# Kernel optimization log

Hardware: AMD Instinct MI355X
Metric: run time of the kernel (lower is better)

## Reference

```python
import jax, jax.numpy as jnp
import numpy as np

DIM = 768
N_HEADS = 12
HEAD_DIM = DIM // N_HEADS
HIDDEN = int(DIM * 4.0)
B, S = 4, 2048
EPS = 1e-6
SCALE = HEAD_DIM ** -0.5


def layer_norm(x, gamma, beta):
    mu = jnp.mean(x, axis=-1, keepdims=True)
    var = jnp.mean((x - mu) ** 2, axis=-1, keepdims=True)
    return (x - mu) * jax.lax.rsqrt(var + EPS) * gamma + beta


def setup_inputs() -> dict:
    key = jax.random.key(0)
    ks = jax.random.split(key, 8)
    x = jax.random.normal(ks[0], (B, S, DIM), dtype=jnp.float32)
    mask = jax.random.randint(ks[1], (B, 1, S, S), 0, 2, dtype=jnp.int32)
    sd = DIM ** -0.5
    return {
        "x": x,
        "mask": mask,
        "w_qkv": jax.random.normal(ks[2], (DIM, 3 * DIM), dtype=jnp.float32) * sd,
        "b_qkv": jnp.zeros((3 * DIM,), jnp.float32),
        "w_proj": jax.random.normal(ks[3], (DIM, DIM), dtype=jnp.float32) * sd,
        "b_proj": jnp.zeros((DIM,), jnp.float32),
        "g1": jnp.ones((DIM,), jnp.float32),
        "beta1": jnp.zeros((DIM,), jnp.float32),
        "g2": jnp.ones((DIM,), jnp.float32),
        "beta2": jnp.zeros((DIM,), jnp.float32),
        "w1": jax.random.normal(ks[4], (DIM, HIDDEN), dtype=jnp.float32) * sd,
        "b1": jnp.zeros((HIDDEN,), jnp.float32),
        "w2": jax.random.normal(ks[5], (HIDDEN, DIM), dtype=jnp.float32) * (HIDDEN ** -0.5),
        "b2": jnp.zeros((DIM,), jnp.float32),
    }


def reference(x, mask, w_qkv, b_qkv, w_proj, b_proj, g1, beta1, g2, beta2, w1, b1, w2, b2):
    # --- attention branch (pre-LN) ---
    h = layer_norm(x, g1, beta1)
    qkv = h @ w_qkv + b_qkv                              # (B,S,3*DIM)
    qkv = qkv.reshape(B, S, 3, N_HEADS, HEAD_DIM)
    q, k, v = (qkv[:, :, 0], qkv[:, :, 1], qkv[:, :, 2])  # (B,S,H,D)
    # scores: (B,H,S,S) -- materialized like the original
    dp = jnp.einsum("bqhd,bkhd->bhqk", q, k) * SCALE
    dp = jnp.where(mask == 0, jnp.float32(-10000.0), dp)
    attn = jax.nn.softmax(dp, axis=-1)
    wa = jnp.einsum("bhqk,bkhd->bqhd", attn, v).reshape(B, S, DIM)
    x = x + (wa @ w_proj + b_proj)
    # --- MLP branch (pre-LN) ---
    h = layer_norm(x, g2, beta2)
    h = jax.nn.gelu(h @ w1 + b1, approximate=False)
    x = x + (h @ w2 + b2)
    return x
```

## Files before the change

kernel.cpp:

```cpp
#include <hip/hip_runtime.h>
#include <hip/hip_bf16.h>
#include <math.h>

typedef __bf16 bf16;
typedef __bf16 bf16x8 __attribute__((ext_vector_type(8)));
typedef short bf16x4s __attribute__((ext_vector_type(4)));
typedef float f32x4 __attribute__((ext_vector_type(4)));

#define DIM 768
#define NH 12
#define HD 64
#define HID 3072
#define BB 4
#define SS 2048
#define SCALE_QK 0.125f
#define QPRESCALE 0.18033688011112042f

#define MFMA(a, b, c) __builtin_amdgcn_mfma_f32_16x16x32_bf16(a, b, c, 0, 0, 0)
#define MFMA16(a, b, c) \
  __builtin_amdgcn_mfma_f32_16x16x16bf16_1k(a, b, c, 0, 0, 0)

__device__ __forceinline__ void gld16(const void* g, void* l) {
  __builtin_amdgcn_global_load_lds(
      (const __attribute__((address_space(1))) void*)g,
      (__attribute__((address_space(3))) void*)l, 16, 0, 0);
}

__device__ __forceinline__ unsigned pk2(float a, float b) {
  union {
    bf16 h[2];
    unsigned u;
  } t;
  t.h[0] = (bf16)a;
  t.h[1] = (bf16)b;
  return t.u;
}

__global__ __launch_bounds__(256) void castT_all_kernel(
    const float* __restrict__ s0, bf16* __restrict__ d0,
    const float* __restrict__ s1, bf16* __restrict__ d1,
    const float* __restrict__ s2, bf16* __restrict__ d2,
    const float* __restrict__ s3, bf16* __restrict__ d3) {
  __shared__ float tile[32][33];
  int id = blockIdx.x;
  const float* in;
  bf16* out;
  int R, C, loc;
  if (id < 1728) { in = s0; out = d0; R = 768; C = 2304; loc = id; }
  else if (id < 2304) { in = s1; out = d1; R = 768; C = 768; loc = id - 1728; }
  else if (id < 4608) { in = s2; out = d2; R = 768; C = 3072; loc = id - 2304; }
  else { in = s3; out = d3; R = 3072; C = 768; loc = id - 4608; }
  const int cb = C >> 5;
  const int c0 = (loc % cb) * 32, r0 = (loc / cb) * 32;
  const int tx = threadIdx.x & 31, ty = threadIdx.x >> 5;
#pragma unroll
  for (int i = 0; i < 32; i += 8)
    tile[ty + i][tx] = in[(size_t)(r0 + ty + i) * C + c0 + tx];
  __syncthreads();
#pragma unroll
  for (int i = 0; i < 32; i += 8)
    out[(size_t)(c0 + ty + i) * R + r0 + tx] = (bf16)tile[tx][ty + i];
}

__global__ __launch_bounds__(256) void maskbits_kernel(
    const int* __restrict__ mask, unsigned* __restrict__ bits) {
  const int i = blockIdx.x * 256 + threadIdx.x;
  unsigned long long m = __ballot(mask[i] != 0);
  const int lane = threadIdx.x & 63;
  if (lane == 0) bits[i >> 5] = (unsigned)m;
  else if (lane == 32) bits[i >> 5] = (unsigned)(m >> 32);
}

__global__ __launch_bounds__(256) void ln_kernel(
    const float* __restrict__ x, const float* __restrict__ g,
    const float* __restrict__ beta, bf16* __restrict__ out) {
  const int row = blockIdx.x, t = threadIdx.x;
  const float* xr = x + (size_t)row * DIM;
  float v0 = xr[t], v1 = xr[t + 256], v2 = xr[t + 512];
  float s = v0 + v1 + v2;
  float s2 = v0 * v0 + v1 * v1 + v2 * v2;
#pragma unroll
  for (int d = 1; d < 64; d <<= 1) {
    s += __shfl_xor(s, d);
    s2 += __shfl_xor(s2, d);
  }
  __shared__ float red[8];
  const int wv = t >> 6, lane = t & 63;
  if (lane == 0) { red[wv] = s; red[wv + 4] = s2; }
  __syncthreads();
  s = red[0] + red[1] + red[2] + red[3];
  s2 = red[4] + red[5] + red[6] + red[7];
  const float mu = s * (1.0f / DIM);
  const float var = s2 * (1.0f / DIM) - mu * mu;
  const float r = rsqrtf(var + 1e-6f);
  bf16* o = out + (size_t)row * DIM;
  o[t] = (bf16)((v0 - mu) * r * g[t] + beta[t]);
  o[t + 256] = (bf16)((v1 - mu) * r * g[t + 256] + beta[t + 256]);
  o[t + 512] = (bf16)((v2 - mu) * r * g[t + 512] + beta[t + 512]);
}

enum { EPI_QKV = 0, EPI_PROJ = 1, EPI_FFN1 = 2, EPI_FFN2 = 3 };

template <int EPI, int K>
__global__ __launch_bounds__(256) void gemm_kernel(
    const bf16* __restrict__ A, const bf16* __restrict__ Bt,
    const float* __restrict__ bias, const float* __restrict__ res,
    void* __restrict__ o0, void* __restrict__ o1, void* __restrict__ o2) {
  __shared__ bf16 As[128 * 64];
  __shared__ bf16 Bs[128 * 64];
  const int tid = threadIdx.x;
  const int wv = tid >> 6, lane = tid & 63;
  const int quad = lane >> 4, l15 = lane & 15;
  const int lrow = lane >> 3, lcol = lane & 7;
  const int m0 = blockIdx.y * 128, n0 = blockIdx.x * 128;
  const int wm = (wv >> 1) * 64, wn = (wv & 1) * 64;

  f32x4 acc[4][4] = {};

  const int swz = (lcol ^ lrow) * 8;
  const bf16* Ag = A + (size_t)(m0 + wv * 32 + lrow) * K + swz;
  const bf16* Bg = Bt + (size_t)(n0 + wv * 32 + lrow) * K + swz;
  bf16* Al = As + (wv * 32) * 64;
  bf16* Bl = Bs + (wv * 32) * 64;

  for (int k0 = 0; k0 < K; k0 += 64) {
#pragma unroll
    for (int i = 0; i < 4; i++) {
      gld16(Ag + (size_t)(i * 8) * K + k0, Al + i * 8 * 64);
      gld16(Bg + (size_t)(i * 8) * K + k0, Bl + i * 8 * 64);
    }
    __syncthreads();
#pragma unroll
    for (int ks = 0; ks < 2; ks++) {
      bf16x8 af[4], bfr[4];
#pragma unroll
      for (int i = 0; i < 4; i++) {
        const int ra = wm + i * 16 + l15;
        af[i] = *(const bf16x8*)&As[ra * 64 + ((ks * 4 + quad) ^ (ra & 7)) * 8];
        const int rb = wn + i * 16 + l15;
        bfr[i] = *(const bf16x8*)&Bs[rb * 64 + ((ks * 4 + quad) ^ (rb & 7)) * 8];
      }
#pragma unroll
      for (int mi = 0; mi < 4; mi++)
#pragma unroll
        for (int ni = 0; ni < 4; ni++)
          acc[mi][ni] = MFMA(af[mi], bfr[ni], acc[mi][ni]);
    }
    __syncthreads();
  }

#pragma unroll
  for (int mi = 0; mi < 4; mi++) {
#pragma unroll
    for (int ni = 0; ni < 4; ni++) {
      const int n = n0 + wn + ni * 16 + l15;
      const float bv = bias[n];
      const int mb = m0 + wm + mi * 16 + quad * 4;
      float val[4];
#pragma unroll
      for (int r = 0; r < 4; r++) val[r] = acc[mi][ni][r] + bv;
      if (EPI == EPI_QKV) {
        const int which = n / 768;
        const int nn = n - which * 768;
        const int hh = nn >> 6, d = nn & 63;
        const int bb = mb >> 11, s = mb & 2047;
        if (which == 0) {
#pragma unroll
          for (int r = 0; r < 4; r++)
            ((bf16*)o0)[((size_t)(bb * NH + hh) * SS + s + r) * HD + d] =
                (bf16)(val[r] * QPRESCALE);
        } else if (which == 1) {
#pragma unroll
          for (int r = 0; r < 4; r++)
            ((bf16*)o1)[((size_t)(bb * NH + hh) * SS + s + r) * HD + d] =
                (bf16)val[r];
        } else {
          uint2 pv;
          pv.x = pk2(val[0], val[1]);
          pv.y = pk2(val[2], val[3]);
          *(uint2*)&((bf16*)o2)[((size_t)(bb * NH + hh) * HD + d) * SS + s] = pv;
        }
      } else if (EPI == EPI_PROJ) {
#pragma unroll
        for (int r = 0; r < 4; r++)
          ((float*)o0)[(size_t)(mb + r) * DIM + n] =
              res[(size_t)(mb + r) * DIM + n] + val[r];
      } else if (EPI == EPI_FFN1) {
#pragma unroll
        for (int r = 0; r < 4; r++) {
          const float ge =
              0.5f * val[r] * (1.0f + erff(val[r] * 0.70710678118654752f));
          ((bf16*)o0)[(size_t)(mb + r) * HID + n] = (bf16)ge;
        }
      } else {
#pragma unroll
        for (int r = 0; r < 4; r++)
          ((float*)o0)[(size_t)(mb + r) * DIM + n] =
              res[(size_t)(mb + r) * DIM + n] + val[r];
      }
    }
  }
}

__global__ __launch_bounds__(256) void attn_kernel(
    const bf16* __restrict__ q, const bf16* __restrict__ k,
    const bf16* __restrict__ vT, const unsigned* __restrict__ bits,
    bf16* __restrict__ wa) {
  const int b = blockIdx.z, h = blockIdx.y, q0 = blockIdx.x * 128;
  const int tid = threadIdx.x, wv = tid >> 6, lane = tid & 63;
  const int quad = lane >> 4, l15 = lane & 15;
  const int lrow = lane >> 3, lcol = lane & 7;

  __shared__ bf16 Ks[64 * 64];
  __shared__ bf16 Vs[64 * 64];

  const bf16* qbh = q + (size_t)(b * NH + h) * SS * HD;
  const bf16* kbh = k + (size_t)(b * NH + h) * SS * HD;
  const bf16* vbh = vT + (size_t)(b * NH + h) * HD * SS;

  bf16x8 aq[2][2];
#pragma unroll
  for (int mi = 0; mi < 2; mi++)
#pragma unroll
    for (int ks = 0; ks < 2; ks++) {
      const int s = q0 + wv * 32 + mi * 16 + l15;
      aq[mi][ks] = *(const bf16x8*)&qbh[(size_t)s * HD + ks * 32 + quad * 8];
    }

  const unsigned long long* mptr[2];
#pragma unroll
  for (int mi = 0; mi < 2; mi++)
    mptr[mi] = (const unsigned long long*)bits +
               (size_t)(b * SS + q0 + wv * 32 + mi * 16 + l15) * 32;

  float lsum[2] = {0.0f, 0.0f};
  f32x4 O[2][4] = {};

  const int swz = (lcol ^ lrow) * 8;

  for (int s0 = 0; s0 < SS; s0 += 64) {
#pragma unroll
    for (int i = 0; i < 2; i++) {
      const int r = wv * 16 + i * 8 + lrow;
      gld16(&kbh[(size_t)(s0 + r) * HD + swz], &Ks[(wv * 16 + i * 8) * 64]);
      gld16(&vbh[(size_t)r * SS + s0 + swz], &Vs[(wv * 16 + i * 8) * 64]);
    }
    const unsigned long long ww[2] = {mptr[0][s0 >> 6] >> (quad * 4),
                                      mptr[1][s0 >> 6] >> (quad * 4)};
    __syncthreads();

    bf16x8 kf[4][2];
#pragma unroll
    for (int ni = 0; ni < 4; ni++)
#pragma unroll
      for (int ks = 0; ks < 2; ks++) {
        const int rr = ni * 16 + l15;
        kf[ni][ks] =
            *(const bf16x8*)&Ks[rr * 64 + ((ks * 4 + quad) ^ (rr & 7)) * 8];
      }
    bf16x4s vf[4][4];
#pragma unroll
    for (int nd = 0; nd < 4; nd++)
#pragma unroll
      for (int ni = 0; ni < 4; ni++) {
        const int row = nd * 16 + l15;
        const int pc = ((ni * 2 + (quad >> 1)) ^ (row & 7));
        vf[nd][ni] =
            *(const bf16x4s*)&Vs[row * 64 + pc * 8 + (quad & 1) * 4];
      }

    unsigned pf[2][4][2];
#pragma unroll
    for (int mi = 0; mi < 2; mi++) {
      const unsigned long long sh = ww[mi];
      float ls = lsum[mi];
#pragma unroll
      for (int ni = 0; ni < 4; ni++) {
        f32x4 a = {};
        a = MFMA(kf[ni][0], aq[mi][0], a);
        a = MFMA(kf[ni][1], aq[mi][1], a);
        float pv[4];
#pragma unroll
        for (int r = 0; r < 4; r++) {
          const unsigned bit = (unsigned)(sh >> (ni * 16 + r)) & 1u;
          const float p = bit ? __builtin_amdgcn_exp2f(a[r]) : 0.0f;
          pv[r] = p;
          ls += p;
        }
        pf[mi][ni][0] = pk2(pv[0], pv[1]);
        pf[mi][ni][1] = pk2(pv[2], pv[3]);
      }
      lsum[mi] = ls;
    }

#pragma unroll
    for (int mi = 0; mi < 2; mi++)
#pragma unroll
      for (int nd = 0; nd < 4; nd++)
#pragma unroll
        for (int ni = 0; ni < 4; ni++) {
          union {
            unsigned u[2];
            bf16x4s v;
          } pp;
          pp.u[0] = pf[mi][ni][0];
          pp.u[1] = pf[mi][ni][1];
          O[mi][nd] = MFMA16(vf[nd][ni], pp.v, O[mi][nd]);
        }
    __syncthreads();
  }

#pragma unroll
  for (int mi = 0; mi < 2; mi++) {
    float ls = lsum[mi];
    ls += __shfl_xor(ls, 16);
    ls += __shfl_xor(ls, 32);
    const float rln = __builtin_amdgcn_rcpf(ls);
    const int s = q0 + wv * 32 + mi * 16 + l15;
    bf16* dst = wa + (size_t)(b * SS + s) * DIM + h * HD + quad * 4;
#pragma unroll
    for (int nd = 0; nd < 4; nd++) {
      uint2 pv;
      pv.x = pk2(O[mi][nd][0] * rln, O[mi][nd][1] * rln);
      pv.y = pk2(O[mi][nd][2] * rln, O[mi][nd][3] * rln);
      *(uint2*)&dst[nd * 16] = pv;
    }
  }
}

extern "C" void kernel_launch(void* const* d_in, const int* in_sizes, int n_in,
                              void* d_out, int out_size, void* d_ws,
                              size_t ws_size, hipStream_t stream) {
  const float* x = (const float*)d_in[0];
  const int* mask = (const int*)d_in[1];
  const float* w_qkv = (const float*)d_in[2];
  const float* b_qkv = (const float*)d_in[3];
  const float* w_proj = (const float*)d_in[4];
  const float* b_proj = (const float*)d_in[5];
  const float* g1 = (const float*)d_in[6];
  const float* beta1 = (const float*)d_in[7];
  const float* g2 = (const float*)d_in[8];
  const float* beta2 = (const float*)d_in[9];
  const float* w1 = (const float*)d_in[10];
  const float* b1 = (const float*)d_in[11];
  const float* w2 = (const float*)d_in[12];
  const float* b2 = (const float*)d_in[13];
  float* out = (float*)d_out;

  char* p = (char*)d_ws;
  auto alloc = [&](size_t bytes) {
    char* r = p;
    p += (bytes + 1023) & ~(size_t)1023;
    return r;
  };
  bf16* wqkvT = (bf16*)alloc((size_t)2304 * 768 * 2);
  bf16* wprojT = (bf16*)alloc((size_t)768 * 768 * 2);
  bf16* w1T = (bf16*)alloc((size_t)3072 * 768 * 2);
  bf16* w2T = (bf16*)alloc((size_t)768 * 3072 * 2);
  unsigned* bits = (unsigned*)alloc((size_t)BB * SS * 64 * 4);
  bf16* h = (bf16*)alloc((size_t)8192 * 768 * 2);
  bf16* qb = (bf16*)alloc((size_t)8192 * 768 * 2);
  bf16* kb = (bf16*)alloc((size_t)8192 * 768 * 2);
  bf16* vtb = (bf16*)alloc((size_t)8192 * 768 * 2);
  bf16* wab = (bf16*)alloc((size_t)8192 * 768 * 2);
  float* x2 = (float*)alloc((size_t)8192 * 768 * 4);
  bf16* ffn1 = (bf16*)alloc((size_t)8192 * 3072 * 2);

  castT_all_kernel<<<6912, 256, 0, stream>>>(w_qkv, wqkvT, w_proj, wprojT, w1,
                                             w1T, w2, w2T);
  maskbits_kernel<<<(BB * SS * SS) / 256, 256, 0, stream>>>(mask, bits);
  ln_kernel<<<8192, 256, 0, stream>>>(x, g1, beta1, h);
  gemm_kernel<EPI_QKV, 768><<<dim3(2304 / 128, 8192 / 128), 256, 0, stream>>>(
      h, wqkvT, b_qkv, nullptr, qb, kb, vtb);
  attn_kernel<<<dim3(SS / 128, NH, BB), 256, 0, stream>>>(qb, kb, vtb, bits, wab);
  gemm_kernel<EPI_PROJ, 768><<<dim3(768 / 128, 8192 / 128), 256, 0, stream>>>(
      wab, wprojT, b_proj, x, x2, nullptr, nullptr);
  ln_kernel<<<8192, 256, 0, stream>>>(x2, g2, beta2, h);
  gemm_kernel<EPI_FFN1, 768><<<dim3(3072 / 128, 8192 / 128), 256, 0, stream>>>(
      h, w1T, b1, nullptr, ffn1, nullptr, nullptr);
  gemm_kernel<EPI_FFN2, 3072><<<dim3(768 / 128, 8192 / 128), 256, 0, stream>>>(
      ffn1, w2T, b2, x2, out, nullptr, nullptr);
}
```

Measured before the change: 497.7 us.

## Shrink attention query tile, compute row sums via MFMA, use 64-wide GEMM tiles

```diff
diff --git a/kernel.cpp b/kernel.cpp
--- a/kernel.cpp
+++ b/kernel.cpp
@@ -13,7 +13,6 @@
 #define HID 3072
 #define BB 4
 #define SS 2048
-#define SCALE_QK 0.125f
 #define QPRESCALE 0.18033688011112042f
 
 #define MFMA(a, b, c) __builtin_amdgcn_mfma_f32_16x16x32_bf16(a, b, c, 0, 0, 0)
@@ -101,47 +100,53 @@
 
 enum { EPI_QKV = 0, EPI_PROJ = 1, EPI_FFN1 = 2, EPI_FFN2 = 3 };
 
-template <int EPI, int K>
+template <int EPI, int K, int TN>
 __global__ __launch_bounds__(256) void gemm_kernel(
     const bf16* __restrict__ A, const bf16* __restrict__ Bt,
     const float* __restrict__ bias, const float* __restrict__ res,
     void* __restrict__ o0, void* __restrict__ o1, void* __restrict__ o2) {
+  constexpr int MI = (TN == 128) ? 4 : 2;
   __shared__ bf16 As[128 * 64];
-  __shared__ bf16 Bs[128 * 64];
+  __shared__ bf16 Bs[TN * 64];
   const int tid = threadIdx.x;
   const int wv = tid >> 6, lane = tid & 63;
   const int quad = lane >> 4, l15 = lane & 15;
   const int lrow = lane >> 3, lcol = lane & 7;
-  const int m0 = blockIdx.y * 128, n0 = blockIdx.x * 128;
-  const int wm = (wv >> 1) * 64, wn = (wv & 1) * 64;
-
-  f32x4 acc[4][4] = {};
+  const int m0 = blockIdx.y * 128, n0 = blockIdx.x * TN;
+  const int wm = (TN == 128) ? (wv >> 1) * 64 : wv * 32;
+  const int wn = (TN == 128) ? (wv & 1) * 64 : 0;
+
+  f32x4 acc[MI][4] = {};
 
   const int swz = (lcol ^ lrow) * 8;
   const bf16* Ag = A + (size_t)(m0 + wv * 32 + lrow) * K + swz;
-  const bf16* Bg = Bt + (size_t)(n0 + wv * 32 + lrow) * K + swz;
+  const bf16* Bg = Bt + (size_t)(n0 + wv * (TN / 4) + lrow) * K + swz;
   bf16* Al = As + (wv * 32) * 64;
-  bf16* Bl = Bs + (wv * 32) * 64;
+  bf16* Bl = Bs + (wv * (TN / 4)) * 64;
 
   for (int k0 = 0; k0 < K; k0 += 64) {
 #pragma unroll
-    for (int i = 0; i < 4; i++) {
+    for (int i = 0; i < 4; i++)
       gld16(Ag + (size_t)(i * 8) * K + k0, Al + i * 8 * 64);
+#pragma unroll
+    for (int i = 0; i < TN / 32; i++)
       gld16(Bg + (size_t)(i * 8) * K + k0, Bl + i * 8 * 64);
-    }
     __syncthreads();
 #pragma unroll
     for (int ks = 0; ks < 2; ks++) {
-      bf16x8 af[4], bfr[4];
-#pragma unroll
-      for (int i = 0; i < 4; i++) {
+      bf16x8 af[MI], bfr[4];
+#pragma unroll
+      for (int i = 0; i < MI; i++) {
         const int ra = wm + i * 16 + l15;
         af[i] = *(const bf16x8*)&As[ra * 64 + ((ks * 4 + quad) ^ (ra & 7)) * 8];
+      }
+#pragma unroll
+      for (int i = 0; i < 4; i++) {
         const int rb = wn + i * 16 + l15;
         bfr[i] = *(const bf16x8*)&Bs[rb * 64 + ((ks * 4 + quad) ^ (rb & 7)) * 8];
       }
 #pragma unroll
-      for (int mi = 0; mi < 4; mi++)
+      for (int mi = 0; mi < MI; mi++)
 #pragma unroll
         for (int ni = 0; ni < 4; ni++)
           acc[mi][ni] = MFMA(af[mi], bfr[ni], acc[mi][ni]);
@@ -150,7 +155,7 @@
   }
 
 #pragma unroll
-  for (int mi = 0; mi < 4; mi++) {
+  for (int mi = 0; mi < MI; mi++) {
 #pragma unroll
     for (int ni = 0; ni < 4; ni++) {
       const int n = n0 + wn + ni * 16 + l15;
@@ -206,36 +211,39 @@
     const bf16* __restrict__ q, const bf16* __restrict__ k,
     const bf16* __restrict__ vT, const unsigned* __restrict__ bits,
     bf16* __restrict__ wa) {
-  const int b = blockIdx.z, h = blockIdx.y, q0 = blockIdx.x * 128;
+  const int b = blockIdx.z, h = blockIdx.y, q0 = blockIdx.x * 64;
   const int tid = threadIdx.x, wv = tid >> 6, lane = tid & 63;
   const int quad = lane >> 4, l15 = lane & 15;
   const int lrow = lane >> 3, lcol = lane & 7;
 
   __shared__ bf16 Ks[64 * 64];
   __shared__ bf16 Vs[64 * 64];
+  __shared__ unsigned lut[32];
+
+  if (tid < 16) {
+    lut[2 * tid] =
+        ((tid & 1) ? 0xFFFFu : 0u) | ((tid & 2) ? 0xFFFF0000u : 0u);
+    lut[2 * tid + 1] =
+        ((tid & 4) ? 0xFFFFu : 0u) | ((tid & 8) ? 0xFFFF0000u : 0u);
+  }
 
   const bf16* qbh = q + (size_t)(b * NH + h) * SS * HD;
   const bf16* kbh = k + (size_t)(b * NH + h) * SS * HD;
   const bf16* vbh = vT + (size_t)(b * NH + h) * HD * SS;
 
-  bf16x8 aq[2][2];
-#pragma unroll
-  for (int mi = 0; mi < 2; mi++)
-#pragma unroll
-    for (int ks = 0; ks < 2; ks++) {
-      const int s = q0 + wv * 32 + mi * 16 + l15;
-      aq[mi][ks] = *(const bf16x8*)&qbh[(size_t)s * HD + ks * 32 + quad * 8];
-    }
-
-  const unsigned long long* mptr[2];
-#pragma unroll
-  for (int mi = 0; mi < 2; mi++)
-    mptr[mi] = (const unsigned long long*)bits +
-               (size_t)(b * SS + q0 + wv * 32 + mi * 16 + l15) * 32;
-
-  float lsum[2] = {0.0f, 0.0f};
-  f32x4 O[2][4] = {};
-
+  const int sq = q0 + wv * 16 + l15;
+  bf16x8 aq[2];
+#pragma unroll
+  for (int ks = 0; ks < 2; ks++)
+    aq[ks] = *(const bf16x8*)&qbh[(size_t)sq * HD + ks * 32 + quad * 8];
+
+  const unsigned long long* mrow =
+      (const unsigned long long*)bits + (size_t)(b * SS + sq) * 32;
+
+  f32x4 O[4] = {};
+  f32x4 lm = {};
+  const short oneb = 0x3F80;
+  const bf16x4s onesA = {oneb, oneb, oneb, oneb};
   const int swz = (lcol ^ lrow) * 8;
 
   for (int s0 = 0; s0 < SS; s0 += 64) {
@@ -245,86 +253,54 @@
       gld16(&kbh[(size_t)(s0 + r) * HD + swz], &Ks[(wv * 16 + i * 8) * 64]);
       gld16(&vbh[(size_t)r * SS + s0 + swz], &Vs[(wv * 16 + i * 8) * 64]);
     }
-    const unsigned long long ww[2] = {mptr[0][s0 >> 6] >> (quad * 4),
-                                      mptr[1][s0 >> 6] >> (quad * 4)};
+    const unsigned long long sh = mrow[s0 >> 6] >> (quad * 4);
+    const unsigned lo32 = (unsigned)sh, hi32 = (unsigned)(sh >> 32);
     __syncthreads();
 
-    bf16x8 kf[4][2];
-#pragma unroll
-    for (int ni = 0; ni < 4; ni++)
-#pragma unroll
-      for (int ks = 0; ks < 2; ks++) {
-        const int rr = ni * 16 + l15;
-        kf[ni][ks] =
-            *(const bf16x8*)&Ks[rr * 64 + ((ks * 4 + quad) ^ (rr & 7)) * 8];
+#pragma unroll
+    for (int ni = 0; ni < 4; ni++) {
+      const int rr = ni * 16 + l15;
+      const bf16x8 kf0 =
+          *(const bf16x8*)&Ks[rr * 64 + (quad ^ (rr & 7)) * 8];
+      const bf16x8 kf1 =
+          *(const bf16x8*)&Ks[rr * 64 + ((4 + quad) ^ (rr & 7)) * 8];
+      f32x4 a = {};
+      a = MFMA(kf0, aq[0], a);
+      a = MFMA(kf1, aq[1], a);
+      const unsigned nib = (ni == 0)   ? (lo32 & 0xF)
+                           : (ni == 1) ? ((lo32 >> 16) & 0xF)
+                           : (ni == 2) ? (hi32 & 0xF)
+                                       : ((hi32 >> 16) & 0xF);
+      const uint2 mw = *(const uint2*)&lut[2 * nib];
+      union {
+        unsigned u[2];
+        bf16x4s v;
+      } pp;
+      pp.u[0] = pk2(__builtin_amdgcn_exp2f(a[0]),
+                    __builtin_amdgcn_exp2f(a[1])) & mw.x;
+      pp.u[1] = pk2(__builtin_amdgcn_exp2f(a[2]),
+                    __builtin_amdgcn_exp2f(a[3])) & mw.y;
+      lm = MFMA16(onesA, pp.v, lm);
+#pragma unroll
+      for (int nd = 0; nd < 4; nd++) {
+        const int row = nd * 16 + l15;
+        const int pc = (ni * 2 + (quad >> 1)) ^ (row & 7);
+        const bf16x4s vf =
+            *(const bf16x4s*)&Vs[row * 64 + pc * 8 + (quad & 1) * 4];
+        O[nd] = MFMA16(vf, pp.v, O[nd]);
       }
-    bf16x4s vf[4][4];
-#pragma unroll
-    for (int nd = 0; nd < 4; nd++)
-#pragma unroll
-      for (int ni = 0; ni < 4; ni++) {
-        const int row = nd * 16 + l15;
-        const int pc = ((ni * 2 + (quad >> 1)) ^ (row & 7));
-        vf[nd][ni] =
-            *(const bf16x4s*)&Vs[row * 64 + pc * 8 + (quad & 1) * 4];
-      }
-
-    unsigned pf[2][4][2];
-#pragma unroll
-    for (int mi = 0; mi < 2; mi++) {
-      const unsigned long long sh = ww[mi];
-      float ls = lsum[mi];
-#pragma unroll
-      for (int ni = 0; ni < 4; ni++) {
-        f32x4 a = {};
-        a = MFMA(kf[ni][0], aq[mi][0], a);
-        a = MFMA(kf[ni][1], aq[mi][1], a);
-        float pv[4];
-#pragma unroll
-        for (int r = 0; r < 4; r++) {
-          const unsigned bit = (unsigned)(sh >> (ni * 16 + r)) & 1u;
-          const float p = bit ? __builtin_amdgcn_exp2f(a[r]) : 0.0f;
-          pv[r] = p;
-          ls += p;
-        }
-        pf[mi][ni][0] = pk2(pv[0], pv[1]);
-        pf[mi][ni][1] = pk2(pv[2], pv[3]);
-      }
-      lsum[mi] = ls;
     }
-
-#pragma unroll
-    for (int mi = 0; mi < 2; mi++)
-#pragma unroll
-      for (int nd = 0; nd < 4; nd++)
-#pragma unroll
-        for (int ni = 0; ni < 4; ni++) {
-          union {
-            unsigned u[2];
-            bf16x4s v;
-          } pp;
-          pp.u[0] = pf[mi][ni][0];
-          pp.u[1] = pf[mi][ni][1];
-          O[mi][nd] = MFMA16(vf[nd][ni], pp.v, O[mi][nd]);
-        }
     __syncthreads();
   }
 
-#pragma unroll
-  for (int mi = 0; mi < 2; mi++) {
-    float ls = lsum[mi];
-    ls += __shfl_xor(ls, 16);
-    ls += __shfl_xor(ls, 32);
-    const float rln = __builtin_amdgcn_rcpf(ls);
-    const int s = q0 + wv * 32 + mi * 16 + l15;
-    bf16* dst = wa + (size_t)(b * SS + s) * DIM + h * HD + quad * 4;
-#pragma unroll
-    for (int nd = 0; nd < 4; nd++) {
-      uint2 pv;
-      pv.x = pk2(O[mi][nd][0] * rln, O[mi][nd][1] * rln);
-      pv.y = pk2(O[mi][nd][2] * rln, O[mi][nd][3] * rln);
-      *(uint2*)&dst[nd * 16] = pv;
-    }
+  const float rln = __builtin_amdgcn_rcpf(lm[0]);
+  bf16* dst = wa + (size_t)(b * SS + sq) * DIM + h * HD + quad * 4;
+#pragma unroll
+  for (int nd = 0; nd < 4; nd++) {
+    uint2 pv;
+    pv.x = pk2(O[nd][0] * rln, O[nd][1] * rln);
+    pv.y = pk2(O[nd][2] * rln, O[nd][3] * rln);
+    *(uint2*)&dst[nd * 16] = pv;
   }
 }
 
@@ -370,14 +346,20 @@
                                              w1T, w2, w2T);
   maskbits_kernel<<<(BB * SS * SS) / 256, 256, 0, stream>>>(mask, bits);
   ln_kernel<<<8192, 256, 0, stream>>>(x, g1, beta1, h);
-  gemm_kernel<EPI_QKV, 768><<<dim3(2304 / 128, 8192 / 128), 256, 0, stream>>>(
-      h, wqkvT, b_qkv, nullptr, qb, kb, vtb);
-  attn_kernel<<<dim3(SS / 128, NH, BB), 256, 0, stream>>>(qb, kb, vtb, bits, wab);
-  gemm_kernel<EPI_PROJ, 768><<<dim3(768 / 128, 8192 / 128), 256, 0, stream>>>(
-      wab, wprojT, b_proj, x, x2, nullptr, nullptr);
+  gemm_kernel<EPI_QKV, 768, 128>
+      <<<dim3(2304 / 128, 8192 / 128), 256, 0, stream>>>(h, wqkvT, b_qkv,
+                                                         nullptr, qb, kb, vtb);
+  attn_kernel<<<dim3(SS / 64, NH, BB), 256, 0, stream>>>(qb, kb, vtb, bits,
+                                                         wab);
+  gemm_kernel<EPI_PROJ, 768, 64>
+      <<<dim3(768 / 64, 8192 / 128), 256, 0, stream>>>(wab, wprojT, b_proj, x,
+                                                       x2, nullptr, nullptr);
   ln_kernel<<<8192, 256, 0, stream>>>(x2, g2, beta2, h);
-  gemm_kernel<EPI_FFN1, 768><<<dim3(3072 / 128, 8192 / 128), 256, 0, stream>>>(
-      h, w1T, b1, nullptr, ffn1, nullptr, nullptr);
-  gemm_kernel<EPI_FFN2, 3072><<<dim3(768 / 128, 8192 / 128), 256, 0, stream>>>(
-      ffn1, w2T, b2, x2, out, nullptr, nullptr);
-}
+  gemm_kernel<EPI_FFN1, 768, 128>
+      <<<dim3(3072 / 128, 8192 / 128), 256, 0, stream>>>(h, w1T, b1, nullptr,
+                                                         ffn1, nullptr,
+                                                         nullptr);
+  gemm_kernel<EPI_FFN2, 3072, 64>
+      <<<dim3(768 / 64, 8192 / 128), 256, 0, stream>>>(ffn1, w2T, b2, x2, out,
+                                                       nullptr, nullptr);
+}
```

Result: no change. 495.2 us (-0.5%).
